# Kernel tuning notes

Measured on AMD Instinct MI355X. Metric: run time of the kernel, lower is better.

The kernel has to match this reference:

```python
import jax, jax.numpy as jnp
import numpy as np

B_, L_, DM = 2, 2048, 1024
DS, DC, EXP, HD = 128, 4, 2, 64
DI = EXP * DM              # 2048
NH = DI // HD              # 32 heads
CONV_DIM = DI + 2 * DS     # 2304
DIN = 2 * DI + 2 * DS + NH # 4384 (z, xBC, dt)
CS = 256                   # SSD chunk size
EPS = 1e-5


def setup_inputs() -> dict:
    key = jax.random.key(0)
    ks = jax.random.split(key, 8)
    s = 0.02
    x = jax.random.normal(ks[0], (B_, L_, DM), jnp.float32)
    norm_w = jnp.ones((DM,), jnp.float32)
    in_proj_w = jax.random.normal(ks[1], (DIN, DM), jnp.float32) * s
    conv_w = jax.random.normal(ks[2], (CONV_DIM, DC), jnp.float32) * 0.2
    conv_b = jnp.zeros((CONV_DIM,), jnp.float32)
    # inverse-softplus of dt ~ U(0.001, 0.1)
    dt_bias = jnp.log(jnp.expm1(jax.random.uniform(ks[3], (NH,), minval=0.001, maxval=0.1)))
    A_log = jnp.log(jax.random.uniform(ks[4], (NH,), minval=1.0, maxval=16.0))
    D = jnp.ones((NH,), jnp.float32)
    gnorm_w = jnp.ones((DI,), jnp.float32)
    out_proj_w = jax.random.normal(ks[5], (DM, DI), jnp.float32) * s
    return dict(x=x, norm_w=norm_w, in_proj_w=in_proj_w, conv_w=conv_w, conv_b=conv_b,
                dt_bias=dt_bias, A_log=A_log, D=D, gnorm_w=gnorm_w, out_proj_w=out_proj_w)


def _segsum(a):
    # a: [..., T] -> [..., T, T]; (i,j) = sum_{j<k<=i} a_k, -inf above diagonal
    T = a.shape[-1]
    cs = jnp.cumsum(a, -1)
    seg = cs[..., :, None] - cs[..., None, :]
    mask = jnp.tril(jnp.ones((T, T), bool))
    return jnp.where(mask, seg, -jnp.inf)


def _ssd(X, A, Bm, Cm):
    # X: [b,l,h,p] (= x*dt), A: [b,l,h] (= dt*a), Bm,Cm: [b,l,n] (ngroups=1)
    b, l, h, p = X.shape
    n, nc = Bm.shape[-1], l // CS
    X = X.reshape(b, nc, CS, h, p)
    A = A.reshape(b, nc, CS, h).transpose(0, 3, 1, 2)  # [b,h,c,s]
    Bm = Bm.reshape(b, nc, CS, n)
    Cm = Cm.reshape(b, nc, CS, n)
    Acs = jnp.cumsum(A, -1)                            # [b,h,c,s]
    Lmat = jnp.exp(_segsum(A))                         # [b,h,c,s,s]
    Y_diag = jnp.einsum('bcln,bcsn,bhcls,bcshp->bclhp', Cm, Bm, Lmat, X)
    decay_states = jnp.exp(Acs[..., -1:] - Acs)        # [b,h,c,s]
    states = jnp.einsum('bcln,bhcl,bclhp->bchpn', Bm, decay_states, X)
    states = jnp.concatenate([jnp.zeros_like(states[:, :1]), states], axis=1)  # [b,c+1,h,p,n]
    decay_chunk = jnp.exp(_segsum(jnp.pad(Acs[..., -1], ((0, 0), (0, 0), (1, 0)))))  # [b,h,c+1,c+1]
    states = jnp.einsum('bhzc,bchpn->bzhpn', decay_chunk, states)[:, :-1]
    Y_off = jnp.einsum('bcln,bchpn,bhcl->bclhp', Cm, states, jnp.exp(Acs))
    return (Y_diag + Y_off).reshape(b, l, h, p)


def _forward(x, norm_w, in_proj_w, conv_w, conv_b, dt_bias, A_log, D, gnorm_w, out_proj_w):
    b, l, _ = x.shape
    # outer RMSNorm
    xn = x * jax.lax.rsqrt(jnp.mean(x * x, -1, keepdims=True) + EPS) * norm_w
    zxbcdt = jnp.einsum('bld,ed->ble', xn, in_proj_w)
    z = zxbcdt[..., :DI]
    xBC = zxbcdt[..., DI:DI + CONV_DIM]
    dt = zxbcdt[..., -NH:]
    # causal depthwise conv1d + bias + silu
    pad = jnp.pad(xBC, ((0, 0), (DC - 1, 0), (0, 0)))
    conv = sum(pad[:, k:k + l, :] * conv_w[:, k] for k in range(DC)) + conv_b
    xBC = conv * jax.nn.sigmoid(conv)
    xs = xBC[..., :DI]
    Bm = xBC[..., DI:DI + DS]
    Cm = xBC[..., DI + DS:]
    dt = jax.nn.softplus(dt + dt_bias)                 # [b,l,h]
    A = -jnp.exp(A_log)                                # [h]
    xh = xs.reshape(b, l, NH, HD)
    y = _ssd(xh * dt[..., None], dt * A, Bm, Cm)
    y = y + D[None, None, :, None] * xh
    y = y.reshape(b, l, DI)
    # gated RMSNorm (norm_before_gate=False): rmsnorm(y * silu(z)) * w
    y = y * (z * jax.nn.sigmoid(z))
    y = y * jax.lax.rsqrt(jnp.mean(y * y, -1, keepdims=True) + EPS) * gnorm_w
    return x + jnp.einsum('bld,ed->ble', y, out_proj_w)


def reference(x, norm_w, in_proj_w, conv_w, conv_b, dt_bias, A_log, D, gnorm_w, out_proj_w):
    return _forward(x, norm_w, in_proj_w, conv_w, conv_b, dt_bias, A_log, D, gnorm_w, out_proj_w)
```

## Files before the change

kernel.cpp:

```cpp
#include <hip/hip_runtime.h>
#include <hip/hip_bf16.h>

#define BB      2
#define LSEQ    2048
#define DMODEL  1024
#define DSTATE  128
#define DCONV   4
#define HEADDIM 64
#define DINNER  2048
#define NHEADS  32
#define CONVD   2304
#define DINP    4384
#define NPAD_IN 4416
#define CHUNK   256
#define NCH     8
#define NROWS   4096
#define EPSF    1e-5f
#define TPAD    264

typedef __attribute__((ext_vector_type(8))) short bf16x8;
typedef __attribute__((ext_vector_type(4))) float f32x4;

#define ASYNC_COPY16(gptr, lptr) \
    __builtin_amdgcn_global_load_lds((const __attribute__((address_space(1))) void*)(gptr), \
                                     (__attribute__((address_space(3))) void*)(lptr), 16, 0, 0)

__device__ __forceinline__ ushort f2bf(float f) {
    __hip_bfloat16 h = __float2bfloat16(f);
    return *(ushort*)&h;
}
__device__ __forceinline__ float bf2f(ushort u) {
    return __uint_as_float(((unsigned)u) << 16);
}
__device__ __forceinline__ short fb(float f) { return (short)f2bf(f); }

__global__ __launch_bounds__(256) void prologue_kernel(
    const float* __restrict__ x, const float* __restrict__ norm_w,
    const float* __restrict__ in_proj_w, const float* __restrict__ out_proj_w,
    const float* __restrict__ gnorm_w,
    ushort* __restrict__ xn_bf, ushort* __restrict__ wi_bf,
    ushort* __restrict__ wo_bf, float* __restrict__ ssq)
{
    int bid = blockIdx.x;
    if (bid < 4416) {
        long i4 = ((long)bid * 256 + threadIdx.x) * 4;
        int n = (int)(i4 >> 10);
        long k = i4 & 1023;
        ushort4 o;
        if (n < DINP) {
            float4 v = *(const float4*)(in_proj_w + ((long)n << 10) + k);
            o.x = f2bf(v.x); o.y = f2bf(v.y); o.z = f2bf(v.z); o.w = f2bf(v.w);
        } else { o.x = o.y = o.z = o.w = 0; }
        *(ushort4*)(wi_bf + i4) = o;
    } else if (bid < 6464) {
        long i4 = ((long)(bid - 4416) * 256 + threadIdx.x) * 4;
        int k = (int)(i4 & 2047);
        float4 v = *(const float4*)(out_proj_w + i4);
        float4 g = *(const float4*)(gnorm_w + k);
        ushort4 o;
        o.x = f2bf(v.x * g.x); o.y = f2bf(v.y * g.y);
        o.z = f2bf(v.z * g.z); o.w = f2bf(v.w * g.w);
        *(ushort4*)(wo_bf + i4) = o;
    } else if (bid < 10560) {
        int row = bid - 6464;
        const float* xr = x + (long)row * DMODEL;
        float4 v = *(const float4*)(xr + threadIdx.x * 4);
        float ss = v.x*v.x + v.y*v.y + v.z*v.z + v.w*v.w;
        for (int off = 32; off; off >>= 1) ss += __shfl_down(ss, off, 64);
        __shared__ float red[4];
        if ((threadIdx.x & 63) == 0) red[threadIdx.x >> 6] = ss;
        __syncthreads();
        float tot = red[0] + red[1] + red[2] + red[3];
        float scale = rsqrtf(tot / (float)DMODEL + EPSF);
        float4 wv = *(const float4*)(norm_w + threadIdx.x * 4);
        ushort4 o;
        o.x = f2bf(v.x * scale * wv.x); o.y = f2bf(v.y * scale * wv.y);
        o.z = f2bf(v.z * scale * wv.z); o.w = f2bf(v.w * scale * wv.w);
        *(ushort4*)(xn_bf + (long)row * DMODEL + threadIdx.x * 4) = o;
    } else {
        ssq[(bid - 10560) * 256 + threadIdx.x] = 0.f;
    }
}

__global__ __launch_bounds__(256, 4) void gemm_bf16_kernel(
    const ushort* __restrict__ A, int lda, long sA,
    const ushort* __restrict__ W, int ldw, long sW,
    void* __restrict__ Cout, int ldc, long sC, int c_bf16,
    const float* __restrict__ resid, const float* __restrict__ rowscale,
    int mtiles, int ntiles, int N, int K)
{
    __shared__ __align__(16) char smem[24576];
    ushort* As = (ushort*)smem;
    ushort* Bs = As + 128 * 64;
    ushort* tu = (ushort*)smem;
    float*  tf = (float*)smem;

    const int t = threadIdx.x;
    const int lane = t & 63;
    const int w = t >> 6;
    const int wm = w & 1, wn = w >> 1;
    const int lm = lane & 15, quad = lane >> 4;

    int pid = blockIdx.x;
    const int GM = 8;
    int width = GM * ntiles;
    int group = pid / width;
    int first_m = group * GM;
    int gsz = mtiles - first_m; if (gsz > GM) gsz = GM;
    int mt = first_m + (pid % width) % gsz;
    int nt = (pid % width) / gsz;
    const int m0 = mt * 128, n0 = nt * 64;

    A += (long)blockIdx.z * sA;
    W += (long)blockIdx.z * sW;

    const ushort* ga[4]; const ushort* gw[2];
#pragma unroll
    for (int i = 0; i < 4; ++i) {
        int s = i * 256 + t;
        int row = s >> 3;
        int kseg = (s & 7) ^ (row & 7);
        ga[i] = A + (long)(m0 + row) * lda + kseg * 8;
    }
#pragma unroll
    for (int i = 0; i < 2; ++i) {
        int s = i * 256 + t;
        int row = s >> 3;
        int kseg = (s & 7) ^ (row & 7);
        gw[i] = W + (long)(n0 + row) * ldw + kseg * 8;
    }

    f32x4 acc[4][2];
    f32x4 zero4 = {0.f, 0.f, 0.f, 0.f};
#pragma unroll
    for (int i = 0; i < 4; ++i) { acc[i][0] = zero4; acc[i][1] = zero4; }

    int arow8[4], arow7[4], brow8[2], brow7[2];
#pragma unroll
    for (int i = 0; i < 4; ++i) {
        int ar = wm * 64 + i * 16 + lm;
        arow8[i] = ar * 8; arow7[i] = ar & 7;
    }
#pragma unroll
    for (int i = 0; i < 2; ++i) {
        int br = wn * 32 + i * 16 + lm;
        brow8[i] = br * 8; brow7[i] = br & 7;
    }

    for (int k0 = 0; k0 < K; k0 += 64) {
#pragma unroll
        for (int i = 0; i < 4; ++i) {
            ASYNC_COPY16(ga[i], &As[(i * 256 + w * 64) * 8]);
            ga[i] += 64;
        }
#pragma unroll
        for (int i = 0; i < 2; ++i) {
            ASYNC_COPY16(gw[i], &Bs[(i * 256 + w * 64) * 8]);
            gw[i] += 64;
        }
        __syncthreads();
#pragma unroll
        for (int ks = 0; ks < 2; ++ks) {
            bf16x8 af[4], bfr[2];
#pragma unroll
            for (int i = 0; i < 4; ++i)
                af[i]  = *(const bf16x8*)&As[(arow8[i] + ((ks * 4 + quad) ^ arow7[i])) * 8];
#pragma unroll
            for (int i = 0; i < 2; ++i)
                bfr[i] = *(const bf16x8*)&Bs[(brow8[i] + ((ks * 4 + quad) ^ brow7[i])) * 8];
#pragma unroll
            for (int im = 0; im < 4; ++im)
#pragma unroll
                for (int in = 0; in < 2; ++in)
                    acc[im][in] = __builtin_amdgcn_mfma_f32_16x16x32_bf16(
                        af[im], bfr[in], acc[im][in], 0, 0, 0);
        }
        __syncthreads();
    }

    if (c_bf16) {
        ushort* C = (ushort*)Cout + (long)blockIdx.z * sC;
#pragma unroll
        for (int mi = 0; mi < 4; ++mi)
#pragma unroll
            for (int ni = 0; ni < 2; ++ni) {
                int c = wn * 32 + ni * 16 + lm;
#pragma unroll
                for (int i = 0; i < 4; ++i) {
                    int r = wm * 64 + mi * 16 + quad * 4 + i;
                    tu[r * 72 + c] = f2bf(acc[mi][ni][i]);
                }
            }
        __syncthreads();
        int r = t >> 1, cb = (t & 1) * 32;
        long rowbase = (long)(m0 + r) * ldc + n0 + cb;
#pragma unroll
        for (int q = 0; q < 4; ++q) {
            int gcol = n0 + cb + q * 8;
            if (gcol < N)
                *(bf16x8*)(C + rowbase + q * 8) =
                    *(const bf16x8*)&tu[r * 72 + cb + q * 8];
        }
    } else {
        float* C = (float*)Cout + (long)blockIdx.z * sC;
#pragma unroll
        for (int p = 0; p < 2; ++p) {
            if (wm == p) {
#pragma unroll
                for (int mi = 0; mi < 4; ++mi)
#pragma unroll
                    for (int i = 0; i < 4; ++i) {
                        int r = mi * 16 + quad * 4 + i;
                        float s = 1.f;
                        if (rowscale)
                            s = rsqrtf(rowscale[m0 + p * 64 + r] * (1.f / (float)DINNER) + EPSF);
#pragma unroll
                        for (int ni = 0; ni < 2; ++ni) {
                            int c = wn * 32 + ni * 16 + lm;
                            tf[r * 68 + c] = acc[mi][ni][i] * s;
                        }
                    }
            }
            __syncthreads();
            int r2 = t >> 2, cb = (t & 3) * 16;
            long gbase = (long)(m0 + p * 64 + r2) * ldc + n0 + cb;
#pragma unroll
            for (int q = 0; q < 4; ++q) {
                float4 v = *(const float4*)&tf[r2 * 68 + cb + q * 4];
                if (resid) {
                    float4 rv = *(const float4*)(resid + gbase + q * 4);
                    v.x += rv.x; v.y += rv.y; v.z += rv.z; v.w += rv.w;
                }
                *(float4*)(C + gbase + q * 4) = v;
            }
            __syncthreads();
        }
    }
}

__global__ __launch_bounds__(256) void conv_acs_kernel(
    const ushort* __restrict__ zx, const float* __restrict__ cw,
    const float* __restrict__ cb, ushort* __restrict__ xBC_bf,
    const float* __restrict__ dt_bias, const float* __restrict__ A_log,
    float* __restrict__ dtv, float* __restrict__ Acs)
{
    int bid = blockIdx.x;
    if (bid < NROWS * 9) {
        int row = bid / 9;
        int c = (bid % 9) * 256 + threadIdx.x;
        int l = row & (LSEQ - 1);
        float acc = cb[c];
#pragma unroll
        for (int k = 0; k < DCONV; ++k) {
            int ls = l + k - (DCONV - 1);
            if (ls >= 0)
                acc += bf2f(zx[(long)(row + k - (DCONV - 1)) * DINP + DINNER + c]) * cw[c * DCONV + k];
        }
        xBC_bf[(long)row * CONVD + c] = f2bf(acc / (1.f + __expf(-acc)));
    } else {
        int idx = bid - NROWS * 9;
        int bc = idx >> 5, h = idx & 31;
        int l = threadIdx.x;
        int row = bc * CHUNK + l;
        float v = bf2f(zx[(long)row * DINP + (DINP - NHEADS) + h]) + dt_bias[h];
        float d = (v > 20.f) ? v : log1pf(__expf(v));
        dtv[row * NHEADS + h] = d;
        float a = -d * __expf(A_log[h]);
        __shared__ float buf[2][CHUNK];
        buf[0][l] = a; __syncthreads();
        int src = 0;
        for (int off = 1; off < CHUNK; off <<= 1) {
            float vv = buf[src][l];
            if (l >= off) vv += buf[src][l - off];
            buf[src ^ 1][l] = vv;
            __syncthreads();
            src ^= 1;
        }
        Acs[(bc * NHEADS + h) * CHUNK + l] = buf[src][l];
    }
}

__global__ __launch_bounds__(256) void prep_b_kernel(
    const ushort* __restrict__ xBC_bf, ushort* __restrict__ Bt)
{
    int bc = blockIdx.x, half = blockIdx.y;
    int t = threadIdx.x;
    int row0 = bc * CHUNK;
    __shared__ ushort tB[64 * TPAD];
    int src_c0 = DINNER + half * 64;
    for (int iter = 0; iter < 8; ++iter) {
        int l = iter * 32 + (t >> 3);
        int cc = (t & 7) * 8;
        ushort u[8];
        *(ushort4*)&u[0] = *(const ushort4*)(xBC_bf + (long)(row0 + l) * CONVD + src_c0 + cc);
        *(ushort4*)&u[4] = *(const ushort4*)(xBC_bf + (long)(row0 + l) * CONVD + src_c0 + cc + 4);
#pragma unroll
        for (int j = 0; j < 8; ++j) tB[(cc + j) * TPAD + l] = u[j];
    }
    __syncthreads();
    int r = t >> 2, seg = (t & 3) * 64;
    ushort* dst = Bt + ((long)bc * DSTATE + half * 64 + r) * CHUNK + seg;
    const ushort* s1 = &tB[r * TPAD + seg];
#pragma unroll
    for (int q = 0; q < 16; ++q)
        *(ushort4*)(dst + q * 4) = *(const ushort4*)(s1 + q * 4);
}

__global__ __launch_bounds__(256) void chunk_state_mfma_kernel(
    const ushort* __restrict__ xBC_bf, const ushort* __restrict__ Bt,
    const float* __restrict__ dtv, const float* __restrict__ acs,
    ushort* __restrict__ state)
{
    int bc = blockIdx.x, h = blockIdx.y;
    int t = threadIdx.x, lane = t & 63, w = t >> 6;
    int lm = lane & 15, quad = lane >> 4;
    int row0 = bc * CHUNK;
    __shared__ ushort xt[64 * TPAD];
    __shared__ float cl[CHUNK];
    {
        float a = acs[(bc * NHEADS + h) * CHUNK + t];
        float T = acs[(bc * NHEADS + h) * CHUNK + CHUNK - 1];
        cl[t] = __expf(T - a) * dtv[(row0 + t) * NHEADS + h];
    }
    __syncthreads();
    for (int iter = 0; iter < 8; ++iter) {
        int l = iter * 32 + (t >> 3);
        int cc = (t & 7) * 8;
        ushort u[8];
        *(ushort4*)&u[0] = *(const ushort4*)(xBC_bf + (long)(row0 + l) * CONVD + h * HEADDIM + cc);
        *(ushort4*)&u[4] = *(const ushort4*)(xBC_bf + (long)(row0 + l) * CONVD + h * HEADDIM + cc + 4);
        float sc = cl[l];
#pragma unroll
        for (int j = 0; j < 8; ++j)
            xt[(cc + j) * TPAD + l] = f2bf(bf2f(u[j]) * sc);
    }
    __syncthreads();

    const ushort* Bb = Bt + (long)bc * DSTATE * CHUNK;
    f32x4 acc[4][2];
    f32x4 zero4 = {0.f, 0.f, 0.f, 0.f};
#pragma unroll
    for (int i = 0; i < 4; ++i) { acc[i][0] = zero4; acc[i][1] = zero4; }

    for (int kt = 0; kt < 8; ++kt) {
        int k = kt * 32 + quad * 8;
        bf16x8 af[4], bfr[2];
#pragma unroll
        for (int mi = 0; mi < 4; ++mi)
            af[mi] = *(const bf16x8*)&xt[(mi * 16 + lm) * TPAD + k];
#pragma unroll
        for (int nj = 0; nj < 2; ++nj)
            bfr[nj] = *(const bf16x8*)(Bb + (long)(w * 32 + nj * 16 + lm) * CHUNK + k);
#pragma unroll
        for (int mi = 0; mi < 4; ++mi)
#pragma unroll
            for (int nj = 0; nj < 2; ++nj)
                acc[mi][nj] = __builtin_amdgcn_mfma_f32_16x16x32_bf16(
                    af[mi], bfr[nj], acc[mi][nj], 0, 0, 0);
    }
    ushort* sp = state + (long)(bc * NHEADS + h) * (DSTATE * HEADDIM);
#pragma unroll
    for (int mi = 0; mi < 4; ++mi)
#pragma unroll
        for (int nj = 0; nj < 2; ++nj) {
            int n = w * 32 + nj * 16 + lm;
#pragma unroll
            for (int i = 0; i < 4; ++i) {
                int p = mi * 16 + quad * 4 + i;
                sp[p * DSTATE + n] = f2bf(acc[mi][nj][i]);
            }
        }
}

__global__ __launch_bounds__(256) void state_scan_kernel(
    ushort* __restrict__ state, const float* __restrict__ Acs)
{
    long flat = (long)blockIdx.x * 256 + threadIdx.x;
    int e = (int)(flat & 8191);
    int bh = (int)(flat >> 13);
    int b = bh >> 5, h = bh & 31;
    float S = 0.f;
    for (int c = 0; c < NCH; ++c) {
        int bc = b * NCH + c;
        long idx = ((long)(bc * NHEADS + h)) * 8192 + e;
        float T = Acs[(bc * NHEADS + h) * CHUNK + CHUNK - 1];
        float tmp = bf2f(state[idx]);
        state[idx] = f2bf(S);
        S = S * __expf(T) + tmp;
    }
}

__global__ __launch_bounds__(256) void ssd_y_mfma_kernel(
    const ushort* __restrict__ xBC_bf, const ushort* __restrict__ G2b,
    const float* __restrict__ acs, const ushort* __restrict__ state,
    const ushort* __restrict__ zxb, const float* __restrict__ dtv,
    const float* __restrict__ Dh, ushort* __restrict__ ybf,
    float* __restrict__ ssq)
{
    int bc = blockIdx.x, h = blockIdx.y;
    int t = threadIdx.x, lane = t & 63, w = t >> 6;
    int lm = lane & 15, quad = lane >> 4;
    int row0 = bc * CHUNK;
    __shared__ ushort xt[64 * TPAD];
    __shared__ float acs_s[CHUNK];
    __shared__ float dl[CHUNK];
    acs_s[t] = acs[(bc * NHEADS + h) * CHUNK + t];
    dl[t] = dtv[(row0 + t) * NHEADS + h];
    __syncthreads();
    for (int iter = 0; iter < 8; ++iter) {
        int l = iter * 32 + (t >> 3);
        int cc = (t & 7) * 8;
        ushort u[8];
        *(ushort4*)&u[0] = *(const ushort4*)(xBC_bf + (long)(row0 + l) * CONVD + h * HEADDIM + cc);
        *(ushort4*)&u[4] = *(const ushort4*)(xBC_bf + (long)(row0 + l) * CONVD + h * HEADDIM + cc + 4);
        float sd = dl[l];
#pragma unroll
        for (int j = 0; j < 8; ++j)
            xt[(cc + j) * TPAD + l] = f2bf(bf2f(u[j]) * sd);
    }
    __syncthreads();

    int lbase = w * 64;
    float acs_l[4], eAl[4];
#pragma unroll
    for (int mi = 0; mi < 4; ++mi) {
        acs_l[mi] = acs_s[lbase + mi * 16 + lm];
        eAl[mi] = __expf(acs_l[mi]);
    }
    f32x4 acc[4][4];
    f32x4 zero4 = {0.f, 0.f, 0.f, 0.f};
#pragma unroll
    for (int i = 0; i < 4; ++i)
#pragma unroll
        for (int j = 0; j < 4; ++j) acc[i][j] = zero4;

    const ushort* g2 = G2b + (long)bc * (CHUNK * CHUNK);

    for (int ks = 0; ks <= 2 * w + 1; ++ks) {
        int sq = ks * 32 + quad * 8;
        bf16x8 bfr[4];
#pragma unroll
        for (int ni = 0; ni < 4; ++ni)
            bfr[ni] = *(const bf16x8*)&xt[(ni * 16 + lm) * TPAD + sq];
        float a8[8];
#pragma unroll
        for (int j = 0; j < 8; ++j) a8[j] = acs_s[sq + j];
#pragma unroll
        for (int mi = 0; mi < 4; ++mi) {
            int lmin = lbase + mi * 16;
            if (ks * 32 > lmin + 15) continue;
            int lv = lmin + lm;
            float al = acs_l[mi];
            bf16x8 g8 = *(const bf16x8*)(g2 + (long)lv * CHUNK + sq);
            bf16x8 af;
#pragma unroll
            for (int j = 0; j < 8; ++j) {
                float v = bf2f((ushort)g8[j]) * __expf(al - a8[j]);
                af[j] = (sq + j > lv) ? (short)0 : fb(v);
            }
#pragma unroll
            for (int ni = 0; ni < 4; ++ni)
                acc[mi][ni] = __builtin_amdgcn_mfma_f32_16x16x32_bf16(
                    af, bfr[ni], acc[mi][ni], 0, 0, 0);
        }
    }

    const ushort* sp = state + (long)(bc * NHEADS + h) * (DSTATE * HEADDIM);
    const ushort* Cb = xBC_bf + (long)row0 * CONVD + DINNER + DSTATE;
    for (int kt = 0; kt < 4; ++kt) {
        int n0 = kt * 32 + quad * 8;
        bf16x8 bfr[4];
#pragma unroll
        for (int ni = 0; ni < 4; ++ni)
            bfr[ni] = *(const bf16x8*)(sp + (long)(ni * 16 + lm) * DSTATE + n0);
#pragma unroll
        for (int mi = 0; mi < 4; ++mi) {
            int lv = lbase + mi * 16 + lm;
            bf16x8 cu = *(const bf16x8*)(Cb + (long)lv * CONVD + n0);
            bf16x8 ce;
            float e = eAl[mi];
#pragma unroll
            for (int j = 0; j < 8; ++j) ce[j] = fb(bf2f((ushort)cu[j]) * e);
#pragma unroll
            for (int ni = 0; ni < 4; ++ni)
                acc[mi][ni] = __builtin_amdgcn_mfma_f32_16x16x32_bf16(
                    ce, bfr[ni], acc[mi][ni], 0, 0, 0);
        }
    }

    float Dv = Dh[h];
#pragma unroll
    for (int mi = 0; mi < 4; ++mi)
#pragma unroll
        for (int i = 0; i < 4; ++i) {
            int l = lbase + mi * 16 + quad * 4 + i;
            long row = row0 + l;
            float ps = 0.f;
#pragma unroll
            for (int ni = 0; ni < 4; ++ni) {
                int p = ni * 16 + lm;
                float xh = bf2f(xBC_bf[row * CONVD + h * HEADDIM + p]);
                float z = bf2f(zxb[row * DINP + h * HEADDIM + p]);
                float o = (acc[mi][ni][i] + Dv * xh) * (z / (1.f + __expf(-z)));
                ps += o * o;
                ybf[row * DINNER + h * HEADDIM + p] = f2bf(o);
            }
#pragma unroll
            for (int m = 1; m < 16; m <<= 1) ps += __shfl_xor(ps, m, 64);
            if (lm == 0) atomicAdd(&ssq[row], ps);
        }
}

extern "C" void kernel_launch(void* const* d_in, const int* in_sizes, int n_in,
                              void* d_out, int out_size, void* d_ws, size_t ws_size,
                              hipStream_t stream)
{
    (void)in_sizes; (void)n_in; (void)out_size; (void)ws_size;
    const float* x          = (const float*)d_in[0];
    const float* norm_w     = (const float*)d_in[1];
    const float* in_proj_w  = (const float*)d_in[2];
    const float* conv_w     = (const float*)d_in[3];
    const float* conv_b     = (const float*)d_in[4];
    const float* dt_bias    = (const float*)d_in[5];
    const float* A_log      = (const float*)d_in[6];
    const float* Dh         = (const float*)d_in[7];
    const float* gnorm_w    = (const float*)d_in[8];
    const float* out_proj_w = (const float*)d_in[9];
    float* out = (float*)d_out;
    float* ws = (float*)d_ws;

    float* zxb_f   = ws;
    float* xbc_f   = zxb_f   + 8978432;
    float* dtv     = xbc_f   + 4718592;
    float* acs     = dtv     + 131072;
    float* g2_f    = acs     + 131072;
    float* state_f = g2_f    + 524288;
    float* bt_f    = state_f + 2097152;
    float* regU    = bt_f    + 262144;
    float* wo_f    = regU    + 4390912;
    float* ssq     = wo_f    + 1048576;

    ushort* zxb_bf = (ushort*)zxb_f;
    ushort* xBC_bf = (ushort*)xbc_f;
    ushort* G2b    = (ushort*)g2_f;
    ushort* state  = (ushort*)state_f;
    ushort* Bt     = (ushort*)bt_f;
    ushort* xn_bf  = (ushort*)regU;
    ushort* wi_bf  = (ushort*)(regU + 2097152);
    ushort* ybf    = (ushort*)regU;
    ushort* wo_bf  = (ushort*)wo_f;

    prologue_kernel<<<dim3(10576), 256, 0, stream>>>(
        x, norm_w, in_proj_w, out_proj_w, gnorm_w, xn_bf, wi_bf, wo_bf, ssq);

    gemm_bf16_kernel<<<dim3(32 * 69), 256, 0, stream>>>(
        xn_bf, DMODEL, 0, wi_bf, DMODEL, 0,
        zxb_bf, DINP, 0, 1, nullptr, nullptr, 32, 69, DINP, DMODEL);

    conv_acs_kernel<<<dim3(NROWS * 9 + BB * NCH * NHEADS), 256, 0, stream>>>(
        zxb_bf, conv_w, conv_b, xBC_bf, dt_bias, A_log, dtv, acs);

    prep_b_kernel<<<dim3(BB * NCH, 2), 256, 0, stream>>>(xBC_bf, Bt);

    gemm_bf16_kernel<<<dim3(8, 1, BB * NCH), 256, 0, stream>>>(
        xBC_bf + DINNER + DSTATE, CONVD, (long)CHUNK * CONVD,
        xBC_bf + DINNER, CONVD, (long)CHUNK * CONVD,
        G2b, CHUNK, (long)CHUNK * CHUNK, 1, nullptr, nullptr, 2, 4, CHUNK, DSTATE);

    chunk_state_mfma_kernel<<<dim3(BB * NCH, NHEADS), 256, 0, stream>>>(
        xBC_bf, Bt, dtv, acs, state);

    state_scan_kernel<<<dim3(BB * NHEADS * 8192 / 256), 256, 0, stream>>>(state, acs);

    ssd_y_mfma_kernel<<<dim3(BB * NCH, NHEADS), 256, 0, stream>>>(
        xBC_bf, G2b, acs, state, zxb_bf, dtv, Dh, ybf, ssq);

    gemm_bf16_kernel<<<dim3(32 * 16), 256, 0, stream>>>(
        ybf, DINNER, 0, wo_bf, DINNER, 0,
        out, DMODEL, 0, 0, x, ssq, 32, 16, DMODEL, DINNER);
}
```

Baseline: 305.6 us.

## Fuse B-transpose into conv kernel, vectorize conv, truncate bf16, factor exps

Moves the B transposition into the conv kernel, where extra blocks recompute the B-segment conv and write the transposed layout directly, which removes one kernel launch. The main conv path now has each thread handle 8 channels with vector loads instead of one channel per thread. Float-to-bf16 conversion in the SSD kernels switches from round-to-nearest to plain truncation. The per-element exp in the diagonal block is factored into a per-row term times per-column terms to cut exp calls, with clamps added for safety. Truncation and the factored exps change numerics slightly, and the B columns of the conv are computed twice.

```diff
diff --git a/kernel.cpp b/kernel.cpp
--- a/kernel.cpp
+++ b/kernel.cpp
@@ -11,7 +11,6 @@
 #define NHEADS  32
 #define CONVD   2304
 #define DINP    4384
-#define NPAD_IN 4416
 #define CHUNK   256
 #define NCH     8
 #define NROWS   4096
@@ -33,6 +32,7 @@
     return __uint_as_float(((unsigned)u) << 16);
 }
 __device__ __forceinline__ short fb(float f) { return (short)f2bf(f); }
+__device__ __forceinline__ short tb(float f) { return (short)(__float_as_uint(f) >> 16); }
 
 __global__ __launch_bounds__(256) void prologue_kernel(
     const float* __restrict__ x, const float* __restrict__ norm_w,
@@ -242,12 +242,53 @@
     const ushort* __restrict__ zx, const float* __restrict__ cw,
     const float* __restrict__ cb, ushort* __restrict__ xBC_bf,
     const float* __restrict__ dt_bias, const float* __restrict__ A_log,
-    float* __restrict__ dtv, float* __restrict__ Acs)
+    float* __restrict__ dtv, float* __restrict__ Acs,
+    ushort* __restrict__ Bt)
 {
+    __shared__ ushort tB[64 * TPAD];
     int bid = blockIdx.x;
-    if (bid < NROWS * 9) {
-        int row = bid / 9;
-        int c = (bid % 9) * 256 + threadIdx.x;
+    int t = threadIdx.x;
+    if (bid < NROWS) {
+        int row = bid;
+        int l = row & (LSEQ - 1);
+        int c = t * 8;
+        float4 cwv[8];
+#pragma unroll
+        for (int j = 0; j < 8; ++j) cwv[j] = *(const float4*)(cw + (c + j) * 4);
+        float acc[8];
+        {
+            float4 b0 = *(const float4*)(cb + c);
+            float4 b1 = *(const float4*)(cb + c + 4);
+            acc[0] = b0.x; acc[1] = b0.y; acc[2] = b0.z; acc[3] = b0.w;
+            acc[4] = b1.x; acc[5] = b1.y; acc[6] = b1.z; acc[7] = b1.w;
+        }
+#pragma unroll
+        for (int k = 0; k < DCONV; ++k) {
+            int ls = l + k - (DCONV - 1);
+            if (ls >= 0) {
+                const ushort* zr = zx + (long)(row + k - (DCONV - 1)) * DINP + DINNER + c;
+                ushort4 a = *(const ushort4*)zr;
+                ushort4 b = *(const ushort4*)(zr + 4);
+                acc[0] += bf2f(a.x) * ((const float*)&cwv[0])[k];
+                acc[1] += bf2f(a.y) * ((const float*)&cwv[1])[k];
+                acc[2] += bf2f(a.z) * ((const float*)&cwv[2])[k];
+                acc[3] += bf2f(a.w) * ((const float*)&cwv[3])[k];
+                acc[4] += bf2f(b.x) * ((const float*)&cwv[4])[k];
+                acc[5] += bf2f(b.y) * ((const float*)&cwv[5])[k];
+                acc[6] += bf2f(b.z) * ((const float*)&cwv[6])[k];
+                acc[7] += bf2f(b.w) * ((const float*)&cwv[7])[k];
+            }
+        }
+        ushort o[8];
+#pragma unroll
+        for (int j = 0; j < 8; ++j)
+            o[j] = f2bf(acc[j] / (1.f + __expf(-acc[j])));
+        ushort* dst = xBC_bf + (long)row * CONVD + c;
+        *(ushort4*)dst = *(ushort4*)&o[0];
+        *(ushort4*)(dst + 4) = *(ushort4*)&o[4];
+    } else if (bid < 2 * NROWS) {
+        int row = bid - NROWS;
+        int c = 2048 + t;
         int l = row & (LSEQ - 1);
         float acc = cb[c];
 #pragma unroll
@@ -257,53 +298,77 @@
                 acc += bf2f(zx[(long)(row + k - (DCONV - 1)) * DINP + DINNER + c]) * cw[c * DCONV + k];
         }
         xBC_bf[(long)row * CONVD + c] = f2bf(acc / (1.f + __expf(-acc)));
-    } else {
-        int idx = bid - NROWS * 9;
+    } else if (bid < 2 * NROWS + BB * NCH * NHEADS) {
+        int idx = bid - 2 * NROWS;
         int bc = idx >> 5, h = idx & 31;
-        int l = threadIdx.x;
+        int l = t;
         int row = bc * CHUNK + l;
         float v = bf2f(zx[(long)row * DINP + (DINP - NHEADS) + h]) + dt_bias[h];
         float d = (v > 20.f) ? v : log1pf(__expf(v));
         dtv[row * NHEADS + h] = d;
         float a = -d * __expf(A_log[h]);
-        __shared__ float buf[2][CHUNK];
-        buf[0][l] = a; __syncthreads();
+        float* buf = (float*)tB;
+        buf[l] = a; __syncthreads();
         int src = 0;
         for (int off = 1; off < CHUNK; off <<= 1) {
-            float vv = buf[src][l];
-            if (l >= off) vv += buf[src][l - off];
-            buf[src ^ 1][l] = vv;
+            float vv = buf[src * CHUNK + l];
+            if (l >= off) vv += buf[src * CHUNK + l - off];
+            buf[(src ^ 1) * CHUNK + l] = vv;
             __syncthreads();
             src ^= 1;
         }
-        Acs[(bc * NHEADS + h) * CHUNK + l] = buf[src][l];
-    }
-}
-
-__global__ __launch_bounds__(256) void prep_b_kernel(
-    const ushort* __restrict__ xBC_bf, ushort* __restrict__ Bt)
-{
-    int bc = blockIdx.x, half = blockIdx.y;
-    int t = threadIdx.x;
-    int row0 = bc * CHUNK;
-    __shared__ ushort tB[64 * TPAD];
-    int src_c0 = DINNER + half * 64;
-    for (int iter = 0; iter < 8; ++iter) {
-        int l = iter * 32 + (t >> 3);
-        int cc = (t & 7) * 8;
-        ushort u[8];
-        *(ushort4*)&u[0] = *(const ushort4*)(xBC_bf + (long)(row0 + l) * CONVD + src_c0 + cc);
-        *(ushort4*)&u[4] = *(const ushort4*)(xBC_bf + (long)(row0 + l) * CONVD + src_c0 + cc + 4);
-#pragma unroll
-        for (int j = 0; j < 8; ++j) tB[(cc + j) * TPAD + l] = u[j];
-    }
-    __syncthreads();
-    int r = t >> 2, seg = (t & 3) * 64;
-    ushort* dst = Bt + ((long)bc * DSTATE + half * 64 + r) * CHUNK + seg;
-    const ushort* s1 = &tB[r * TPAD + seg];
-#pragma unroll
-    for (int q = 0; q < 16; ++q)
-        *(ushort4*)(dst + q * 4) = *(const ushort4*)(s1 + q * 4);
+        Acs[(bc * NHEADS + h) * CHUNK + l] = buf[src * CHUNK + l];
+    } else {
+        int idx = bid - (2 * NROWS + BB * NCH * NHEADS);
+        int bc = idx >> 1, half = idx & 1;
+        int row0 = bc * CHUNK;
+        int cc8 = (t & 7) * 8;
+        int cxbc = 2048 + half * 64 + cc8;
+        float4 cwv[8];
+#pragma unroll
+        for (int j = 0; j < 8; ++j) cwv[j] = *(const float4*)(cw + (cxbc + j) * 4);
+        float cb0[8];
+        {
+            float4 b0 = *(const float4*)(cb + cxbc);
+            float4 b1 = *(const float4*)(cb + cxbc + 4);
+            cb0[0] = b0.x; cb0[1] = b0.y; cb0[2] = b0.z; cb0[3] = b0.w;
+            cb0[4] = b1.x; cb0[5] = b1.y; cb0[6] = b1.z; cb0[7] = b1.w;
+        }
+        for (int iter = 0; iter < 8; ++iter) {
+            int l = iter * 32 + (t >> 3);
+            int row = row0 + l;
+            float acc[8];
+#pragma unroll
+            for (int j = 0; j < 8; ++j) acc[j] = cb0[j];
+#pragma unroll
+            for (int k = 0; k < DCONV; ++k) {
+                int ls = l + k - (DCONV - 1);
+                if (ls >= 0) {
+                    const ushort* zr = zx + (long)(row + k - (DCONV - 1)) * DINP + DINNER + cxbc;
+                    ushort4 a = *(const ushort4*)zr;
+                    ushort4 b = *(const ushort4*)(zr + 4);
+                    acc[0] += bf2f(a.x) * ((const float*)&cwv[0])[k];
+                    acc[1] += bf2f(a.y) * ((const float*)&cwv[1])[k];
+                    acc[2] += bf2f(a.z) * ((const float*)&cwv[2])[k];
+                    acc[3] += bf2f(a.w) * ((const float*)&cwv[3])[k];
+                    acc[4] += bf2f(b.x) * ((const float*)&cwv[4])[k];
+                    acc[5] += bf2f(b.y) * ((const float*)&cwv[5])[k];
+                    acc[6] += bf2f(b.z) * ((const float*)&cwv[6])[k];
+                    acc[7] += bf2f(b.w) * ((const float*)&cwv[7])[k];
+                }
+            }
+#pragma unroll
+            for (int j = 0; j < 8; ++j)
+                tB[(cc8 + j) * TPAD + l] = (ushort)tb(acc[j] / (1.f + __expf(-acc[j])));
+        }
+        __syncthreads();
+        int r = t >> 2, seg = (t & 3) * 64;
+        ushort* dst = Bt + ((long)bc * DSTATE + half * 64 + r) * CHUNK + seg;
+        const ushort* s1 = &tB[r * TPAD + seg];
+#pragma unroll
+        for (int q = 0; q < 16; ++q)
+            *(ushort4*)(dst + q * 4) = *(const ushort4*)(s1 + q * 4);
+    }
 }
 
 __global__ __launch_bounds__(256) void chunk_state_mfma_kernel(
@@ -332,7 +397,7 @@
         float sc = cl[l];
 #pragma unroll
         for (int j = 0; j < 8; ++j)
-            xt[(cc + j) * TPAD + l] = f2bf(bf2f(u[j]) * sc);
+            xt[(cc + j) * TPAD + l] = (ushort)tb(bf2f(u[j]) * sc);
     }
     __syncthreads();
 
@@ -416,7 +481,7 @@
         float sd = dl[l];
 #pragma unroll
         for (int j = 0; j < 8; ++j)
-            xt[(cc + j) * TPAD + l] = f2bf(bf2f(u[j]) * sd);
+            xt[(cc + j) * TPAD + l] = (ushort)tb(bf2f(u[j]) * sd);
     }
     __syncthreads();
 
@@ -442,21 +507,24 @@
 #pragma unroll
         for (int ni = 0; ni < 4; ++ni)
             bfr[ni] = *(const bf16x8*)&xt[(ni * 16 + lm) * TPAD + sq];
-        float a8[8];
-#pragma unroll
-        for (int j = 0; j < 8; ++j) a8[j] = acs_s[sq + j];
+        float base = acs_s[sq];
+        float e8[8];
+        e8[0] = 1.f;
+#pragma unroll
+        for (int j = 1; j < 8; ++j)
+            e8[j] = __expf(fminf(base - acs_s[sq + j], 80.f));
 #pragma unroll
         for (int mi = 0; mi < 4; ++mi) {
             int lmin = lbase + mi * 16;
             if (ks * 32 > lmin + 15) continue;
             int lv = lmin + lm;
-            float al = acs_l[mi];
+            float em = __expf(fminf(acs_l[mi] - base, 0.f));
             bf16x8 g8 = *(const bf16x8*)(g2 + (long)lv * CHUNK + sq);
             bf16x8 af;
 #pragma unroll
             for (int j = 0; j < 8; ++j) {
-                float v = bf2f((ushort)g8[j]) * __expf(al - a8[j]);
-                af[j] = (sq + j > lv) ? (short)0 : fb(v);
+                float v = bf2f((ushort)g8[j]) * (em * e8[j]);
+                af[j] = (sq + j > lv) ? (short)0 : tb(v);
             }
 #pragma unroll
             for (int ni = 0; ni < 4; ++ni)
@@ -480,7 +548,7 @@
             bf16x8 ce;
             float e = eAl[mi];
 #pragma unroll
-            for (int j = 0; j < 8; ++j) ce[j] = fb(bf2f((ushort)cu[j]) * e);
+            for (int j = 0; j < 8; ++j) ce[j] = tb(bf2f((ushort)cu[j]) * e);
 #pragma unroll
             for (int ni = 0; ni < 4; ++ni)
                 acc[mi][ni] = __builtin_amdgcn_mfma_f32_16x16x32_bf16(
@@ -557,10 +625,8 @@
         xn_bf, DMODEL, 0, wi_bf, DMODEL, 0,
         zxb_bf, DINP, 0, 1, nullptr, nullptr, 32, 69, DINP, DMODEL);
 
-    conv_acs_kernel<<<dim3(NROWS * 9 + BB * NCH * NHEADS), 256, 0, stream>>>(
-        zxb_bf, conv_w, conv_b, xBC_bf, dt_bias, A_log, dtv, acs);
-
-    prep_b_kernel<<<dim3(BB * NCH, 2), 256, 0, stream>>>(xBC_bf, Bt);
+    conv_acs_kernel<<<dim3(2 * NROWS + BB * NCH * NHEADS + BB * NCH * 2), 256, 0, stream>>>(
+        zxb_bf, conv_w, conv_b, xBC_bf, dt_bias, A_log, dtv, acs, Bt);
 
     gemm_bf16_kernel<<<dim3(8, 1, BB * NCH), 256, 0, stream>>>(
         xBC_bf + DINNER + DSTATE, CONVD, (long)CHUNK * CONVD,
```

Result: no change. 305.0 us (-0.2%).
